# Kernel optimization log

Measured on AMD Instinct MI355X. Metric: run time of the kernel, lower is better.

## Reference

```python
import jax, jax.numpy as jnp
import numpy as np


def setup_inputs() -> dict:
    key = jax.random.key(0)
    k1, k2, k3, k4 = jax.random.split(key, 4)
    B, S, E, D = 8, 2048, 1024, 64
    return {
        "sequence": jax.random.normal(k1, (B, S, E), dtype=jnp.float32),
        "Wk": jax.random.normal(k2, (E, D), dtype=jnp.float32) * (E ** -0.5),
        "Wq": jax.random.normal(k3, (E, D), dtype=jnp.float32) * (E ** -0.5),
        "Wv": jax.random.normal(k4, (E, D), dtype=jnp.float32) * (E ** -0.5),
    }


def reference(sequence, Wk, Wq, Wv):
    # sequence: [B, S, E]; Wk/Wq/Wv: [E, D]
    B, S, E = sequence.shape
    D = Wk.shape[-1]
    k = sequence @ Wk  # [B, S, D]
    q = sequence @ Wq  # [B, S, D]
    v = sequence @ Wv  # [B, S, D]
    scores = jnp.einsum("bqd,bkd->bqk", q, k) * (D ** -0.5)  # [B, S, S]
    causal = jnp.tril(jnp.ones((S, S), dtype=bool))
    scores = jnp.where(causal, scores, -jnp.inf)
    attn = jax.nn.softmax(scores, axis=-1)  # [B, S, S]
    out = jnp.einsum("bqk,bkd->bqd", attn, v)  # [B, S, D]
    return (out, attn)
```

## Files before the change

kernel.cpp:

```cpp
#include <hip/hip_runtime.h>
#include <hip/hip_bf16.h>


typedef __attribute__((ext_vector_type(8))) __bf16 bf16x8;
typedef __attribute__((ext_vector_type(4))) float f32x4;

constexpr int S_LEN = 2048;

__device__ inline unsigned short f2bf(float f) {
  union { float f; unsigned u; } v; v.f = f;
  unsigned u = v.u + 0x7FFFu + ((v.u >> 16) & 1u);
  return (unsigned short)(u >> 16);
}

__device__ inline bf16x8 pack8(float4 f0, float4 f1) {
  union { __hip_bfloat162 h[4]; bf16x8 v; } u;
  u.h[0] = __float22bfloat162_rn(float2{f0.x, f0.y});
  u.h[1] = __float22bfloat162_rn(float2{f0.z, f0.w});
  u.h[2] = __float22bfloat162_rn(float2{f1.x, f1.y});
  u.h[3] = __float22bfloat162_rn(float2{f1.z, f1.w});
  return u.v;
}

__global__ __launch_bounds__(256) void wt_conv(
    const float* __restrict__ Wq, const float* __restrict__ Wk,
    const float* __restrict__ Wv, unsigned short* __restrict__ wt) {
  __shared__ float T[64][65];
  const int mat = blockIdx.y;
  const int k0 = blockIdx.x * 64;
  const float* W = (mat == 0) ? Wq : ((mat == 1) ? Wk : Wv);
  const int t = threadIdx.x;

  for (int s = 0; s < 4; ++s) {
    int rr = (t >> 4) + s * 16;
    int cc = (t & 15) * 4;
    float4 f = *(const float4*)(W + (size_t)(k0 + rr) * 64 + cc);
    T[rr][cc] = f.x; T[rr][cc + 1] = f.y; T[rr][cc + 2] = f.z; T[rr][cc + 3] = f.w;
  }
  __syncthreads();
  const float sc = (mat == 0) ? 0.125f : 1.0f;
  const int n = t >> 2, kc = (t & 3) * 16;
  union { unsigned short s[16]; uint4 v[2]; } tmp;
  for (int i = 0; i < 16; ++i) tmp.s[i] = f2bf(T[kc + i][n] * sc);
  unsigned short* dst = wt + (size_t)(mat * 64 + n) * 1024 + k0 + kc;
  *(uint4*)dst = tmp.v[0];
  *(uint4*)(dst + 8) = tmp.v[1];
}

__global__ __launch_bounds__(256) void qkv_gemm(
    const float* __restrict__ seq, const unsigned short* __restrict__ wt,
    unsigned short* __restrict__ qb, unsigned short* __restrict__ kb,
    unsigned short* __restrict__ vt) {
  __shared__ float Red[2][6][16][17];
  const int row0 = blockIdx.x * 16;
  const int t = threadIdx.x;
  const int wv = t >> 6, lane = t & 63, lm = lane & 15, lq = lane >> 4;
  const int kh = wv >> 1, ng = wv & 1;

  f32x4 acc[6];
  for (int i = 0; i < 6; ++i) acc[i] = (f32x4){0.f, 0.f, 0.f, 0.f};

  const float* ap = seq + (size_t)(row0 + lm) * 1024 + kh * 512 + lq * 8;
  const unsigned short* bp = wt + (size_t)(ng * 96 + lm) * 1024 + kh * 512 + lq * 8;

  for (int i = 0; i < 16; ++i) {
    float4 f0 = *(const float4*)(ap + i * 32);
    float4 f1 = *(const float4*)(ap + i * 32 + 4);
    bf16x8 a = pack8(f0, f1);
    for (int nt = 0; nt < 6; ++nt) {
      bf16x8 bfr = *(const bf16x8*)(bp + (size_t)nt * 16 * 1024 + i * 32);
      acc[nt] = __builtin_amdgcn_mfma_f32_16x16x32_bf16(a, bfr, acc[nt], 0, 0, 0);
    }
  }

  if (kh == 1) {
    for (int nt = 0; nt < 6; ++nt)
      for (int r = 0; r < 4; ++r)
        Red[ng][nt][lq * 4 + r][lm] = acc[nt][r];
  }
  __syncthreads();
  if (kh == 0) {
    const int b = row0 >> 11, s0 = row0 & (S_LEN - 1);
    for (int nt = 0; nt < 6; ++nt) {
      float v[4];
      for (int r = 0; r < 4; ++r) v[r] = acc[nt][r] + Red[ng][nt][lq * 4 + r][lm];
      int n = ng * 96 + nt * 16 + lm;
      if (n < 128) {
        unsigned short* dst = (n < 64) ? qb : kb;
        for (int r = 0; r < 4; ++r)
          dst[(size_t)(row0 + lq * 4 + r) * 64 + (n & 63)] = f2bf(v[r]);
      } else {
        int d = n - 128;
        ushort4 u;
        u.x = f2bf(v[0]); u.y = f2bf(v[1]); u.z = f2bf(v[2]); u.w = f2bf(v[3]);
        *(ushort4*)(vt + ((size_t)(b * 64 + d)) * S_LEN + s0 + lq * 4) = u;
      }
    }
  }
}

__global__ __launch_bounds__(64) void attn_stats(
    const unsigned short* __restrict__ qb, const unsigned short* __restrict__ kb,
    float* __restrict__ lbuf) {
  const int q0 = blockIdx.x * 16, c0 = blockIdx.y * 512, b = blockIdx.z;
  if (c0 >= q0 + 16) return;
  const int kend = min(c0 + 512, q0 + 16);
  const int lane = threadIdx.x, lm = lane & 15, lq = lane >> 4;

  const unsigned short* qp = qb + ((size_t)(b * S_LEN + q0 + lm)) * 64 + lq * 8;
  bf16x8 qf0 = *(const bf16x8*)qp;
  bf16x8 qf1 = *(const bf16x8*)(qp + 32);
  const int row = q0 + lq * 4;

  float lp[4] = {0.f, 0.f, 0.f, 0.f};
  for (int kk = c0; kk < kend; kk += 32) {
    for (int tile = 0; tile < 2; ++tile) {
      int key = kk + tile * 16 + lm;
      const unsigned short* kp =
          kb + ((size_t)(b * S_LEN + kk + tile * 16 + lm)) * 64 + lq * 8;
      f32x4 z = (f32x4){0.f, 0.f, 0.f, 0.f};
      z = __builtin_amdgcn_mfma_f32_16x16x32_bf16(qf0, *(const bf16x8*)kp, z, 0, 0, 0);
      z = __builtin_amdgcn_mfma_f32_16x16x32_bf16(qf1, *(const bf16x8*)(kp + 32), z, 0, 0, 0);
      for (int r = 0; r < 4; ++r)
        if (key <= row + r) lp[r] += __expf(z[r]);
    }
  }
  for (int off = 1; off < 16; off <<= 1)
    for (int r = 0; r < 4; ++r) lp[r] += __shfl_xor(lp[r], off);
  if (lm == 0)
    for (int r = 0; r < 4; ++r)
      unsafeAtomicAdd(&lbuf[b * S_LEN + q0 + lq * 4 + r], lp[r]);
}

__global__ __launch_bounds__(64) void attn_write(
    const unsigned short* __restrict__ qb, const unsigned short* __restrict__ kb,
    const unsigned short* __restrict__ vt, const float* __restrict__ lbuf,
    float* __restrict__ outp, float* __restrict__ attnp) {
  __shared__ unsigned short Ps[16][40];
  const int q0 = blockIdx.x * 16, c0 = blockIdx.y * 256, b = blockIdx.z;
  const int lane = threadIdx.x, lm = lane & 15, lq = lane >> 4;
  float* arow = attnp + (size_t)b * S_LEN * S_LEN;

  if (c0 >= q0 + 16) {
    float4 z4 = {0.f, 0.f, 0.f, 0.f};
    for (int r = 0; r < 16; ++r)
      *(float4*)(arow + (size_t)(q0 + r) * S_LEN + c0 + lane * 4) = z4;
    return;
  }

  const unsigned short* qp = qb + ((size_t)(b * S_LEN + q0 + lm)) * 64 + lq * 8;
  bf16x8 qf0 = *(const bf16x8*)qp;
  bf16x8 qf1 = *(const bf16x8*)(qp + 32);
  const int row = q0 + lq * 4;

  float il[4];
  for (int r = 0; r < 4; ++r) il[r] = 1.0f / lbuf[b * S_LEN + q0 + lq * 4 + r];

  f32x4 o[4];
  for (int i = 0; i < 4; ++i) o[i] = (f32x4){0.f, 0.f, 0.f, 0.f};

  for (int kk = c0; kk < c0 + 256; kk += 32) {
    if (kk >= q0 + 16) {
      int rr = lane >> 3, cc = (lane & 7) * 4;
      float4 z4 = {0.f, 0.f, 0.f, 0.f};
      *(float4*)(arow + (size_t)(q0 + rr) * S_LEN + kk + cc) = z4;
      *(float4*)(arow + (size_t)(q0 + 8 + rr) * S_LEN + kk + cc) = z4;
      continue;
    }
    f32x4 c2[2];
    for (int tile = 0; tile < 2; ++tile) {
      const unsigned short* kp =
          kb + ((size_t)(b * S_LEN + kk + tile * 16 + lm)) * 64 + lq * 8;
      f32x4 z = (f32x4){0.f, 0.f, 0.f, 0.f};
      z = __builtin_amdgcn_mfma_f32_16x16x32_bf16(qf0, *(const bf16x8*)kp, z, 0, 0, 0);
      z = __builtin_amdgcn_mfma_f32_16x16x32_bf16(qf1, *(const bf16x8*)(kp + 32), z, 0, 0, 0);
      c2[tile] = z;
    }
    for (int tile = 0; tile < 2; ++tile) {
      int key = kk + tile * 16 + lm;
      for (int r = 0; r < 4; ++r) {
        float p = (key > row + r) ? 0.f : __expf(c2[tile][r]) * il[r];
        arow[(size_t)(q0 + lq * 4 + r) * S_LEN + key] = p;
        Ps[lq * 4 + r][tile * 16 + lm] = f2bf(p);
      }
    }
    bf16x8 pa = *(const bf16x8*)&Ps[lm][lq * 8];
    for (int nt = 0; nt < 4; ++nt) {
      const unsigned short* vp =
          vt + ((size_t)(b * 64 + nt * 16 + lm)) * S_LEN + kk + lq * 8;
      o[nt] = __builtin_amdgcn_mfma_f32_16x16x32_bf16(pa, *(const bf16x8*)vp, o[nt], 0, 0, 0);
    }
  }

  for (int nt = 0; nt < 4; ++nt)
    for (int r = 0; r < 4; ++r)
      unsafeAtomicAdd(outp + ((size_t)(b * S_LEN + q0 + lq * 4 + r)) * 64 + nt * 16 + lm,
                      o[nt][r]);
}

extern "C" void kernel_launch(void* const* d_in, const int* in_sizes, int n_in,
                              void* d_out, int out_size, void* d_ws, size_t ws_size,
                              hipStream_t stream) {
  const float* seq = (const float*)d_in[0];
  const float* Wk  = (const float*)d_in[1];
  const float* Wq  = (const float*)d_in[2];
  const float* Wv  = (const float*)d_in[3];

  float* outp = (float*)d_out;
  float* attnp = outp + (size_t)8 * S_LEN * 64;

  unsigned short* qb = (unsigned short*)d_ws;
  unsigned short* kb = qb + (size_t)16384 * 64;
  unsigned short* vt = kb + (size_t)16384 * 64;
  unsigned short* wt = vt + (size_t)8 * 64 * S_LEN;
  float* lbuf = (float*)(wt + (size_t)192 * 1024);

  hipMemsetAsync(lbuf, 0, (size_t)16384 * 4, stream);
  hipMemsetAsync(outp, 0, (size_t)8 * S_LEN * 64 * 4, stream);

  wt_conv<<<dim3(16, 3), 256, 0, stream>>>(Wq, Wk, Wv, wt);
  qkv_gemm<<<dim3(1024, 1), 256, 0, stream>>>(seq, wt, qb, kb, vt);
  attn_stats<<<dim3(128, 4, 8), 64, 0, stream>>>(qb, kb, lbuf);
  attn_write<<<dim3(128, 8, 8), 64, 0, stream>>>(qb, kb, vt, lbuf, outp, attnp);
}
```

Before: 299.2 us.

## Enlarge tiles and stage K and sequence tiles in LDS across all kernels

The QKV GEMM now processes 64 rows per block, staging bf16-converted sequence tiles in shared memory so each loaded weight fragment feeds four MFMA row tiles. The stats and write kernels move from 16-query single-wave blocks to 64-query four-wave blocks that share K tiles loaded once into LDS. This cuts redundant global loads of K and weights, at the cost of extra barriers, larger LDS use and fewer blocks per launch. The zero-fill of the masked region is also reorganised per wave.

```diff
diff --git a/kernel.cpp b/kernel.cpp
--- a/kernel.cpp
+++ b/kernel.cpp
@@ -13,8 +13,8 @@
   return (unsigned short)(u >> 16);
 }
 
-__device__ inline bf16x8 pack8(float4 f0, float4 f1) {
-  union { __hip_bfloat162 h[4]; bf16x8 v; } u;
+__device__ inline uint4 pack8u(float4 f0, float4 f1) {
+  union { __hip_bfloat162 h[4]; uint4 v; } u;
   u.h[0] = __float22bfloat162_rn(float2{f0.x, f0.y});
   u.h[1] = __float22bfloat162_rn(float2{f0.z, f0.w});
   u.h[2] = __float22bfloat162_rn(float2{f1.x, f1.y});
@@ -51,150 +51,180 @@
     const float* __restrict__ seq, const unsigned short* __restrict__ wt,
     unsigned short* __restrict__ qb, unsigned short* __restrict__ kb,
     unsigned short* __restrict__ vt) {
-  __shared__ float Red[2][6][16][17];
-  const int row0 = blockIdx.x * 16;
+  __shared__ unsigned short As[64][72];
+  const int row0 = blockIdx.x * 64;
   const int t = threadIdx.x;
   const int wv = t >> 6, lane = t & 63, lm = lane & 15, lq = lane >> 4;
-  const int kh = wv >> 1, ng = wv & 1;
-
-  f32x4 acc[6];
-  for (int i = 0; i < 6; ++i) acc[i] = (f32x4){0.f, 0.f, 0.f, 0.f};
-
-  const float* ap = seq + (size_t)(row0 + lm) * 1024 + kh * 512 + lq * 8;
-  const unsigned short* bp = wt + (size_t)(ng * 96 + lm) * 1024 + kh * 512 + lq * 8;
+
+  f32x4 acc[12];
+  for (int i = 0; i < 12; ++i) acc[i] = (f32x4){0.f, 0.f, 0.f, 0.f};
+
+  const int srow = t >> 2, skc = (t & 3) * 16;
 
   for (int i = 0; i < 16; ++i) {
-    float4 f0 = *(const float4*)(ap + i * 32);
-    float4 f1 = *(const float4*)(ap + i * 32 + 4);
-    bf16x8 a = pack8(f0, f1);
-    for (int nt = 0; nt < 6; ++nt) {
-      bf16x8 bfr = *(const bf16x8*)(bp + (size_t)nt * 16 * 1024 + i * 32);
-      acc[nt] = __builtin_amdgcn_mfma_f32_16x16x32_bf16(a, bfr, acc[nt], 0, 0, 0);
-    }
-  }
-
-  if (kh == 1) {
-    for (int nt = 0; nt < 6; ++nt)
-      for (int r = 0; r < 4; ++r)
-        Red[ng][nt][lq * 4 + r][lm] = acc[nt][r];
-  }
-  __syncthreads();
-  if (kh == 0) {
-    const int b = row0 >> 11, s0 = row0 & (S_LEN - 1);
-    for (int nt = 0; nt < 6; ++nt) {
-      float v[4];
-      for (int r = 0; r < 4; ++r) v[r] = acc[nt][r] + Red[ng][nt][lq * 4 + r][lm];
-      int n = ng * 96 + nt * 16 + lm;
-      if (n < 128) {
-        unsigned short* dst = (n < 64) ? qb : kb;
-        for (int r = 0; r < 4; ++r)
-          dst[(size_t)(row0 + lq * 4 + r) * 64 + (n & 63)] = f2bf(v[r]);
-      } else {
-        int d = n - 128;
+    __syncthreads();
+    const float* src = seq + (size_t)(row0 + srow) * 1024 + i * 64 + skc;
+    float4 f0 = *(const float4*)src;
+    float4 f1 = *(const float4*)(src + 4);
+    float4 f2 = *(const float4*)(src + 8);
+    float4 f3 = *(const float4*)(src + 12);
+    *(uint4*)&As[srow][skc] = pack8u(f0, f1);
+    *(uint4*)&As[srow][skc + 8] = pack8u(f2, f3);
+    __syncthreads();
+    for (int ks = 0; ks < 2; ++ks) {
+      bf16x8 a[4];
+      for (int mt = 0; mt < 4; ++mt)
+        a[mt] = *(const bf16x8*)&As[mt * 16 + lm][ks * 32 + lq * 8];
+      for (int nt = 0; nt < 3; ++nt) {
+        const unsigned short* bp =
+            wt + (size_t)(wv * 48 + nt * 16 + lm) * 1024 + i * 64 + ks * 32 + lq * 8;
+        bf16x8 bfr = *(const bf16x8*)bp;
+        for (int mt = 0; mt < 4; ++mt)
+          acc[mt * 3 + nt] =
+              __builtin_amdgcn_mfma_f32_16x16x32_bf16(a[mt], bfr, acc[mt * 3 + nt], 0, 0, 0);
+      }
+    }
+  }
+
+  const int bb = row0 >> 11;
+  const int s0 = row0 & (S_LEN - 1);
+  for (int nt = 0; nt < 3; ++nt) {
+    int ng = wv * 48 + nt * 16 + lm;
+    int mat = ng >> 6, d = ng & 63;
+    for (int mt = 0; mt < 4; ++mt) {
+      f32x4 v = acc[mt * 3 + nt];
+      if (mat == 2) {
         ushort4 u;
         u.x = f2bf(v[0]); u.y = f2bf(v[1]); u.z = f2bf(v[2]); u.w = f2bf(v[3]);
-        *(ushort4*)(vt + ((size_t)(b * 64 + d)) * S_LEN + s0 + lq * 4) = u;
-      }
-    }
-  }
-}
-
-__global__ __launch_bounds__(64) void attn_stats(
+        *(ushort4*)(vt + ((size_t)(bb * 64 + d)) * S_LEN + s0 + mt * 16 + lq * 4) = u;
+      } else {
+        unsigned short* dst = mat ? kb : qb;
+        for (int r = 0; r < 4; ++r)
+          dst[(size_t)(row0 + mt * 16 + lq * 4 + r) * 64 + d] = f2bf(v[r]);
+      }
+    }
+  }
+}
+
+__global__ __launch_bounds__(256) void attn_stats(
     const unsigned short* __restrict__ qb, const unsigned short* __restrict__ kb,
     float* __restrict__ lbuf) {
-  const int q0 = blockIdx.x * 16, c0 = blockIdx.y * 512, b = blockIdx.z;
-  if (c0 >= q0 + 16) return;
-  const int kend = min(c0 + 512, q0 + 16);
-  const int lane = threadIdx.x, lm = lane & 15, lq = lane >> 4;
-
-  const unsigned short* qp = qb + ((size_t)(b * S_LEN + q0 + lm)) * 64 + lq * 8;
+  __shared__ unsigned short Ks[128][72];
+  const int q0 = blockIdx.x * 64, c0 = blockIdx.y * 1024, b = blockIdx.z;
+  if (c0 >= q0 + 64) return;
+  const int kend = min(c0 + 1024, q0 + 64);
+  const int t = threadIdx.x, wv = t >> 6, lane = t & 63, lm = lane & 15, lq = lane >> 4;
+
+  const unsigned short* qp = qb + ((size_t)(b * S_LEN + q0 + wv * 16 + lm)) * 64 + lq * 8;
   bf16x8 qf0 = *(const bf16x8*)qp;
   bf16x8 qf1 = *(const bf16x8*)(qp + 32);
-  const int row = q0 + lq * 4;
+  const int rw0 = q0 + wv * 16;
 
   float lp[4] = {0.f, 0.f, 0.f, 0.f};
-  for (int kk = c0; kk < kend; kk += 32) {
-    for (int tile = 0; tile < 2; ++tile) {
-      int key = kk + tile * 16 + lm;
-      const unsigned short* kp =
-          kb + ((size_t)(b * S_LEN + kk + tile * 16 + lm)) * 64 + lq * 8;
-      f32x4 z = (f32x4){0.f, 0.f, 0.f, 0.f};
-      z = __builtin_amdgcn_mfma_f32_16x16x32_bf16(qf0, *(const bf16x8*)kp, z, 0, 0, 0);
-      z = __builtin_amdgcn_mfma_f32_16x16x32_bf16(qf1, *(const bf16x8*)(kp + 32), z, 0, 0, 0);
-      for (int r = 0; r < 4; ++r)
-        if (key <= row + r) lp[r] += __expf(z[r]);
+  const int srow = t >> 1, shalf = (t & 1) * 32;
+
+  for (int kk = c0; kk < kend; kk += 128) {
+    __syncthreads();
+    const unsigned short* src = kb + ((size_t)(b * S_LEN + kk + srow)) * 64 + shalf;
+    for (int j = 0; j < 4; ++j)
+      *(uint4*)&Ks[srow][shalf + j * 8] = *(const uint4*)(src + j * 8);
+    __syncthreads();
+    if (kk <= rw0 + 15) {
+      int ktmax = min(8, (rw0 + 15 - kk) / 16 + 1);
+      for (int kt = 0; kt < ktmax; ++kt) {
+        int key = kk + kt * 16 + lm;
+        f32x4 z = (f32x4){0.f, 0.f, 0.f, 0.f};
+        bf16x8 k0 = *(const bf16x8*)&Ks[kt * 16 + lm][lq * 8];
+        bf16x8 k1 = *(const bf16x8*)&Ks[kt * 16 + lm][32 + lq * 8];
+        z = __builtin_amdgcn_mfma_f32_16x16x32_bf16(qf0, k0, z, 0, 0, 0);
+        z = __builtin_amdgcn_mfma_f32_16x16x32_bf16(qf1, k1, z, 0, 0, 0);
+        for (int r = 0; r < 4; ++r) {
+          float e = __expf(z[r]);
+          lp[r] += (key <= rw0 + lq * 4 + r) ? e : 0.f;
+        }
+      }
     }
   }
   for (int off = 1; off < 16; off <<= 1)
     for (int r = 0; r < 4; ++r) lp[r] += __shfl_xor(lp[r], off);
   if (lm == 0)
     for (int r = 0; r < 4; ++r)
-      unsafeAtomicAdd(&lbuf[b * S_LEN + q0 + lq * 4 + r], lp[r]);
-}
-
-__global__ __launch_bounds__(64) void attn_write(
+      unsafeAtomicAdd(&lbuf[b * S_LEN + rw0 + lq * 4 + r], lp[r]);
+}
+
+__global__ __launch_bounds__(256) void attn_write(
     const unsigned short* __restrict__ qb, const unsigned short* __restrict__ kb,
     const unsigned short* __restrict__ vt, const float* __restrict__ lbuf,
     float* __restrict__ outp, float* __restrict__ attnp) {
-  __shared__ unsigned short Ps[16][40];
-  const int q0 = blockIdx.x * 16, c0 = blockIdx.y * 256, b = blockIdx.z;
-  const int lane = threadIdx.x, lm = lane & 15, lq = lane >> 4;
+  __shared__ unsigned short Ks[256][72];
+  __shared__ unsigned short Ps[4][16][72];
+  const int q0 = blockIdx.x * 64, c0 = blockIdx.y * 256, b = blockIdx.z;
+  const int t = threadIdx.x, wv = t >> 6, lane = t & 63, lm = lane & 15, lq = lane >> 4;
   float* arow = attnp + (size_t)b * S_LEN * S_LEN;
 
-  if (c0 >= q0 + 16) {
+  if (c0 >= q0 + 64) {
+    const int col = (t & 63) * 4, r0 = t >> 6;
     float4 z4 = {0.f, 0.f, 0.f, 0.f};
-    for (int r = 0; r < 16; ++r)
-      *(float4*)(arow + (size_t)(q0 + r) * S_LEN + c0 + lane * 4) = z4;
+    for (int rr = r0; rr < 64; rr += 4)
+      *(float4*)(arow + (size_t)(q0 + rr) * S_LEN + c0 + col) = z4;
     return;
   }
 
-  const unsigned short* qp = qb + ((size_t)(b * S_LEN + q0 + lm)) * 64 + lq * 8;
+  {
+    const unsigned short* src = kb + ((size_t)(b * S_LEN + c0 + t)) * 64;
+    for (int j = 0; j < 8; ++j)
+      *(uint4*)&Ks[t][j * 8] = *(const uint4*)(src + j * 8);
+  }
+  const unsigned short* qp = qb + ((size_t)(b * S_LEN + q0 + wv * 16 + lm)) * 64 + lq * 8;
   bf16x8 qf0 = *(const bf16x8*)qp;
   bf16x8 qf1 = *(const bf16x8*)(qp + 32);
-  const int row = q0 + lq * 4;
+  const int rw0 = q0 + wv * 16;
 
   float il[4];
-  for (int r = 0; r < 4; ++r) il[r] = 1.0f / lbuf[b * S_LEN + q0 + lq * 4 + r];
+  for (int r = 0; r < 4; ++r) il[r] = 1.0f / lbuf[b * S_LEN + rw0 + lq * 4 + r];
 
   f32x4 o[4];
   for (int i = 0; i < 4; ++i) o[i] = (f32x4){0.f, 0.f, 0.f, 0.f};
-
-  for (int kk = c0; kk < c0 + 256; kk += 32) {
-    if (kk >= q0 + 16) {
-      int rr = lane >> 3, cc = (lane & 7) * 4;
-      float4 z4 = {0.f, 0.f, 0.f, 0.f};
-      *(float4*)(arow + (size_t)(q0 + rr) * S_LEN + kk + cc) = z4;
-      *(float4*)(arow + (size_t)(q0 + 8 + rr) * S_LEN + kk + cc) = z4;
+  __syncthreads();
+
+  for (int st = 0; st < 4; ++st) {
+    const int kk0 = c0 + st * 64;
+    if (kk0 > rw0 + 15) {
+      for (int rr = 0; rr < 16; ++rr)
+        arow[(size_t)(rw0 + rr) * S_LEN + kk0 + lane] = 0.f;
       continue;
     }
-    f32x4 c2[2];
-    for (int tile = 0; tile < 2; ++tile) {
-      const unsigned short* kp =
-          kb + ((size_t)(b * S_LEN + kk + tile * 16 + lm)) * 64 + lq * 8;
+    f32x4 c4[4];
+    for (int kt = 0; kt < 4; ++kt) {
       f32x4 z = (f32x4){0.f, 0.f, 0.f, 0.f};
-      z = __builtin_amdgcn_mfma_f32_16x16x32_bf16(qf0, *(const bf16x8*)kp, z, 0, 0, 0);
-      z = __builtin_amdgcn_mfma_f32_16x16x32_bf16(qf1, *(const bf16x8*)(kp + 32), z, 0, 0, 0);
-      c2[tile] = z;
-    }
-    for (int tile = 0; tile < 2; ++tile) {
-      int key = kk + tile * 16 + lm;
+      bf16x8 k0 = *(const bf16x8*)&Ks[st * 64 + kt * 16 + lm][lq * 8];
+      bf16x8 k1 = *(const bf16x8*)&Ks[st * 64 + kt * 16 + lm][32 + lq * 8];
+      z = __builtin_amdgcn_mfma_f32_16x16x32_bf16(qf0, k0, z, 0, 0, 0);
+      z = __builtin_amdgcn_mfma_f32_16x16x32_bf16(qf1, k1, z, 0, 0, 0);
+      c4[kt] = z;
+    }
+    for (int kt = 0; kt < 4; ++kt) {
+      int key = kk0 + kt * 16 + lm;
       for (int r = 0; r < 4; ++r) {
-        float p = (key > row + r) ? 0.f : __expf(c2[tile][r]) * il[r];
-        arow[(size_t)(q0 + lq * 4 + r) * S_LEN + key] = p;
-        Ps[lq * 4 + r][tile * 16 + lm] = f2bf(p);
-      }
-    }
-    bf16x8 pa = *(const bf16x8*)&Ps[lm][lq * 8];
-    for (int nt = 0; nt < 4; ++nt) {
-      const unsigned short* vp =
-          vt + ((size_t)(b * 64 + nt * 16 + lm)) * S_LEN + kk + lq * 8;
-      o[nt] = __builtin_amdgcn_mfma_f32_16x16x32_bf16(pa, *(const bf16x8*)vp, o[nt], 0, 0, 0);
+        int rw = rw0 + lq * 4 + r;
+        float p = (key > rw) ? 0.f : __expf(c4[kt][r]) * il[r];
+        arow[(size_t)rw * S_LEN + key] = p;
+        Ps[wv][lq * 4 + r][kt * 16 + lm] = f2bf(p);
+      }
+    }
+    for (int ks2 = 0; ks2 < 2; ++ks2) {
+      bf16x8 pa = *(const bf16x8*)&Ps[wv][lm][ks2 * 32 + lq * 8];
+      for (int nt = 0; nt < 4; ++nt) {
+        const unsigned short* vp =
+            vt + ((size_t)(b * 64 + nt * 16 + lm)) * S_LEN + kk0 + ks2 * 32 + lq * 8;
+        o[nt] = __builtin_amdgcn_mfma_f32_16x16x32_bf16(pa, *(const bf16x8*)vp, o[nt], 0, 0, 0);
+      }
     }
   }
 
   for (int nt = 0; nt < 4; ++nt)
     for (int r = 0; r < 4; ++r)
-      unsafeAtomicAdd(outp + ((size_t)(b * S_LEN + q0 + lq * 4 + r)) * 64 + nt * 16 + lm,
+      unsafeAtomicAdd(outp + ((size_t)(b * S_LEN + rw0 + lq * 4 + r)) * 64 + nt * 16 + lm,
                       o[nt][r]);
 }
 
@@ -219,7 +249,7 @@
   hipMemsetAsync(outp, 0, (size_t)8 * S_LEN * 64 * 4, stream);
 
   wt_conv<<<dim3(16, 3), 256, 0, stream>>>(Wq, Wk, Wv, wt);
-  qkv_gemm<<<dim3(1024, 1), 256, 0, stream>>>(seq, wt, qb, kb, vt);
-  attn_stats<<<dim3(128, 4, 8), 64, 0, stream>>>(qb, kb, lbuf);
-  attn_write<<<dim3(128, 8, 8), 64, 0, stream>>>(qb, kb, vt, lbuf, outp, attnp);
-}
+  qkv_gemm<<<dim3(256, 1), 256, 0, stream>>>(seq, wt, qb, kb, vt);
+  attn_stats<<<dim3(32, 2, 8), 256, 0, stream>>>(qb, kb, lbuf);
+  attn_write<<<dim3(32, 8, 8), 256, 0, stream>>>(qb, kb, vt, lbuf, outp, attnp);
+}
```

New measurement: 253.7 us. -15.2%, faster.
